# Kernel optimization log

Measured on AMD Instinct MI355X. Metric: run time of the kernel, lower is better.

The kernel has to match this reference:

```python
import jax, jax.numpy as jnp
import numpy as np

BATCH, T, D_MODEL, DIM = 8, 4096, 512, 512
R_MIN, R_MAX, MAX_PHASE = 0.0, 1.0, 6.28


def setup_inputs() -> dict:
    key = jax.random.key(0)
    ks = jax.random.split(key, 8)
    x = jax.random.normal(ks[0], (BATCH, T, D_MODEL), dtype=jnp.float32)
    h0 = jnp.zeros((BATCH, 1, DIM), dtype=jnp.float32)
    # nu_log / theta_log per the module's initializers
    u1 = jax.random.uniform(ks[1], (DIM,))
    nu_log = jnp.log(-0.5 * jnp.log(u1 * (R_MAX ** 2 - R_MIN ** 2) + R_MIN ** 2)).astype(jnp.float32)
    u2 = jax.random.uniform(ks[2], (DIM,))
    theta_log = jnp.log(MAX_PHASE * u2).astype(jnp.float32)
    # B ~ N(0,1)/sqrt(2*D_in), C ~ N(0,1)/sqrt(D_out)
    B_re = (jax.random.normal(ks[3], (D_MODEL, DIM)) / jnp.sqrt(2.0 * D_MODEL)).astype(jnp.float32)
    B_im = (jax.random.normal(ks[4], (D_MODEL, DIM)) / jnp.sqrt(2.0 * D_MODEL)).astype(jnp.float32)
    C_re = (jax.random.normal(ks[5], (DIM, D_MODEL)) / jnp.sqrt(float(D_MODEL))).astype(jnp.float32)
    C_im = (jax.random.normal(ks[6], (DIM, D_MODEL)) / jnp.sqrt(float(D_MODEL))).astype(jnp.float32)
    D_param = jax.random.normal(ks[7], (D_MODEL,)).astype(jnp.float32)
    # gamma_log = log(sqrt(1 - |Lambda|^2)) with Lambda from nu/theta
    diag_lambda = jnp.exp(-jnp.exp(nu_log) + 1j * jnp.exp(theta_log))
    gamma_log = jnp.log(jnp.sqrt(1.0 - jnp.abs(diag_lambda) ** 2)).astype(jnp.float32)
    return {"x": x, "h0": h0, "nu_log": nu_log, "theta_log": theta_log,
            "B_re": B_re, "B_im": B_im, "C_re": C_re, "C_im": C_im,
            "D_param": D_param, "gamma_log": gamma_log}


def _binary_op(ei, ej):
    a_i, b_i = ei
    a_j, b_j = ej
    return (a_j * a_i, a_j * b_i + b_j)


def reference(x, h0, nu_log, theta_log, B_re, B_im, C_re, C_im, D_param, gamma_log):
    B, T_len, _ = x.shape
    Lambda = jnp.exp(-jnp.exp(nu_log) + 1j * jnp.exp(theta_log))            # (N,) complex
    B_norm = (B_re + 1j * B_im) * jnp.exp(gamma_log)[None, :]               # (D,N) complex
    C = C_re + 1j * C_im                                                     # (N,D) complex
    # Input projection: Bu[b,t,n] = sum_d x[b,t,d] * B_norm[d,n]
    Bu = jnp.einsum('btd,dn->btn', x.astype(jnp.complex64), B_norm)
    Bu = jnp.concatenate([h0.astype(jnp.complex64), Bu], axis=1)             # (B,T+1,N)
    Lam = jnp.broadcast_to(Lambda, Bu.shape)                                 # (B,T+1,N)
    _, H = jax.lax.associative_scan(_binary_op, (Lam, Bu), axis=1)
    H = H[:, 1:]                                                             # (B,T,N)
    y = jnp.einsum('btn,nd->btd', H, C).real + D_param * x                   # (B,T,D)
    new_h = H[:, -1:]                                                        # (B,1,N) complex
    return (y, new_h)
```

## Files before the change

kernel.cpp:

```cpp
#include <hip/hip_runtime.h>

#define T_LEN 4096
#define DMODEL 512
#define DIM 512
#define NBATCH 8
#define MROWS (NBATCH * T_LEN)
#define NCHUNK 128
#define LCHUNK 32

typedef __attribute__((ext_vector_type(8))) short short8;
typedef __attribute__((ext_vector_type(4))) float float4v;

__device__ __forceinline__ ushort f2b(float f) {
    union { float fl; unsigned u; } v; v.fl = f;
    unsigned u = v.u;
    return (ushort)((u + 0x7FFFu + ((u >> 16) & 1u)) >> 16);
}
__device__ __forceinline__ float b2f(ushort u) {
    union { unsigned u; float f; } v; v.u = (unsigned)u << 16; return v.f;
}

__device__ __forceinline__ void glds16(const ushort* g, ushort* l) {
    __builtin_amdgcn_global_load_lds(
        (const __attribute__((address_space(1))) void*)g,
        (__attribute__((address_space(3))) void*)l, 16, 0, 0);
}

#define XBLK (MROWS * 512 / 4 / 256)
#define BBLK (1024 * 512 / 256)
#define CBLK (512 * 1024 / 256)

__global__ __launch_bounds__(256) void k_prep(const float* __restrict__ x,
                                              const float* __restrict__ B_re,
                                              const float* __restrict__ B_im,
                                              const float* __restrict__ gamma_log,
                                              const float* __restrict__ C_re,
                                              const float* __restrict__ C_im,
                                              ushort* __restrict__ Xb,
                                              ushort* __restrict__ BT,
                                              ushort* __restrict__ CT) {
    int bb = blockIdx.x;
    if (bb < XBLK) {
        int i = (bb * 256 + threadIdx.x) * 4;
        float4 v = *(const float4*)(x + i);
        ushort4 o;
        o.x = f2b(v.x); o.y = f2b(v.y); o.z = f2b(v.z); o.w = f2b(v.w);
        *(ushort4*)(Xb + i) = o;
    } else if (bb < XBLK + BBLK) {
        int idx = (bb - XBLK) * 256 + threadIdx.x;
        int n = idx >> 9;
        int d = idx & 511;
        float v;
        if (n < 512) v = B_re[d * 512 + n] * __expf(gamma_log[n]);
        else { int nn = n - 512; v = B_im[d * 512 + nn] * __expf(gamma_log[nn]); }
        BT[idx] = f2b(v);
    } else {
        int idx = (bb - XBLK - BBLK) * 256 + threadIdx.x;
        int d = idx >> 10;
        int k = idx & 1023;
        float v = (k < 512) ? C_re[k * 512 + d] : -C_im[(k - 512) * 512 + d];
        CT[idx] = f2b(v);
    }
}

template<int K, int MODE, int NBN>
__global__ __launch_bounds__(256) void k_gemm(
    const ushort* __restrict__ A, const ushort* __restrict__ Bt,
    ushort* __restrict__ oRe, ushort* __restrict__ oIm,
    float* __restrict__ y, const float* __restrict__ x, const float* __restrict__ Dp) {
    __shared__ ushort sA[128 * 64];
    __shared__ ushort sB[128 * 64];
    const int tid = threadIdx.x;
    const int L = blockIdx.x;
    const int xcd = L & 7;
    const int slot = L >> 3;
    const int m0 = (xcd * 32 + slot / NBN) * 128;
    const int n0 = (slot % NBN) * 128;
    const int wave = tid >> 6;
    const int lane = tid & 63;
    const int wm = (wave >> 1) * 64;
    const int wn = (wave & 1) * 64;
    const int lr = lane & 15;
    const int quad = lane >> 4;

    const int srow = lane >> 3;
    const int schunk = (lane & 7) ^ srow;
    const ushort* gA0 = A + (size_t)(m0 + wave * 32 + srow) * K + schunk * 8;
    const ushort* gB0 = Bt + (size_t)(n0 + wave * 32 + srow) * K + schunk * 8;

    float4v acc[4][4];
#pragma unroll
    for (int i = 0; i < 4; i++)
#pragma unroll
        for (int j = 0; j < 4; j++) {
            float4v z = {0.f, 0.f, 0.f, 0.f};
            acc[i][j] = z;
        }

    for (int k0 = 0; k0 < K; k0 += 64) {
        __syncthreads();
#pragma unroll
        for (int c = 0; c < 4; c++) {
            glds16(gA0 + (size_t)(c * 8) * K + k0, &sA[(wave * 32 + c * 8) * 64]);
            glds16(gB0 + (size_t)(c * 8) * K + k0, &sB[(wave * 32 + c * 8) * 64]);
        }
        __syncthreads();

#pragma unroll
        for (int kk = 0; kk < 2; kk++) {
            short8 af[4], bfr[4];
#pragma unroll
            for (int i = 0; i < 4; i++) {
                int row = wm + i * 16 + lr;
                af[i] = *(const short8*)&sA[row * 64 + (((kk * 4 + quad) ^ (row & 7)) * 8)];
            }
#pragma unroll
            for (int j = 0; j < 4; j++) {
                int row = wn + j * 16 + lr;
                bfr[j] = *(const short8*)&sB[row * 64 + (((kk * 4 + quad) ^ (row & 7)) * 8)];
            }
#pragma unroll
            for (int i = 0; i < 4; i++)
#pragma unroll
                for (int j = 0; j < 4; j++)
                    acc[i][j] = __builtin_amdgcn_mfma_f32_16x16x32_bf16(af[i], bfr[j], acc[i][j], 0, 0, 0);
        }
    }

#pragma unroll
    for (int i = 0; i < 4; i++) {
#pragma unroll
        for (int j = 0; j < 4; j++) {
            int gmb = m0 + wm + i * 16 + quad * 4;
            int gn = n0 + wn + j * 16 + lr;
#pragma unroll
            for (int r = 0; r < 4; r++) {
                float v = acc[i][j][r];
                int row = gmb + r;
                if (MODE == 1) {
                    if (gn < 512) oRe[(size_t)row * 512 + gn] = f2b(v);
                    else oIm[(size_t)row * 512 + (gn - 512)] = f2b(v);
                } else {
                    size_t o = (size_t)row * 512 + gn;
                    y[o] = v + Dp[gn] * x[o];
                }
            }
        }
    }
}


__device__ __forceinline__ void lambda_of(const float* nu_log, const float* theta_log,
                                          int n, float& lre, float& lim) {
    float e = __expf(nu_log[n]);
    float th = __expf(theta_log[n]);
    float rad = __expf(-e);
    float s, c;
    __sincosf(th, &s, &c);
    lre = rad * c;
    lim = rad * s;
}

__global__ __launch_bounds__(256) void k_scan1(const ushort* __restrict__ BuRe,
                                               const ushort* __restrict__ BuIm,
                                               const float* __restrict__ nu_log,
                                               const float* __restrict__ theta_log,
                                               float* __restrict__ cRe, float* __restrict__ cIm) {
    int n2 = threadIdx.x;
    int b = blockIdx.x >> 7;
    int c = blockIdx.x & 127;
    float lre0, lim0, lre1, lim1;
    lambda_of(nu_log, theta_log, 2 * n2, lre0, lim0);
    lambda_of(nu_log, theta_log, 2 * n2 + 1, lre1, lim1);
    float hr0 = 0.f, hi0 = 0.f, hr1 = 0.f, hi1 = 0.f;
    size_t base = ((size_t)b * T_LEN + (size_t)c * LCHUNK) * 512 + 2 * n2;
#pragma unroll 8
    for (int j = 0; j < LCHUNK; j++) {
        ushort2 ur = *(const ushort2*)(BuRe + base + (size_t)j * 512);
        ushort2 ui = *(const ushort2*)(BuIm + base + (size_t)j * 512);
        float br0 = b2f(ur.x), br1 = b2f(ur.y), bi0 = b2f(ui.x), bi1 = b2f(ui.y);
        float nr0 = lre0 * hr0 - lim0 * hi0 + br0;
        float ni0 = lre0 * hi0 + lim0 * hr0 + bi0;
        hr0 = nr0; hi0 = ni0;
        float nr1 = lre1 * hr1 - lim1 * hi1 + br1;
        float ni1 = lre1 * hi1 + lim1 * hr1 + bi1;
        hr1 = nr1; hi1 = ni1;
    }
    size_t co = ((size_t)b * NCHUNK + c) * 512 + 2 * n2;
    *(float2*)(cRe + co) = make_float2(hr0, hr1);
    *(float2*)(cIm + co) = make_float2(hi0, hi1);
}

__global__ __launch_bounds__(64) void k_scan2(const float* __restrict__ cRe,
                                              const float* __restrict__ cIm,
                                              const float* __restrict__ h0,
                                              const float* __restrict__ nu_log,
                                              const float* __restrict__ theta_log,
                                              float* __restrict__ pRe, float* __restrict__ pIm,
                                              float* __restrict__ newH, int newh_mode) {
    int idx = blockIdx.x * 64 + threadIdx.x;
    int b = idx >> 9;
    int n = idx & 511;
    float lre, lim;
    lambda_of(nu_log, theta_log, n, lre, lim);
    float Lr = lre, Li = lim;
#pragma unroll
    for (int s = 0; s < 5; s++) {
        float nr = Lr * Lr - Li * Li;
        float ni = 2.f * Lr * Li;
        Lr = nr; Li = ni;
    }
    float cr = h0[b * 512 + n];
    float ci = 0.f;
#pragma unroll 4
    for (int c = 0; c < NCHUNK; c++) {
        size_t o = ((size_t)b * NCHUNK + c) * 512 + n;
        pRe[o] = cr;
        pIm[o] = ci;
        float ar = cRe[o], ai = cIm[o];
        float nr = Lr * cr - Li * ci + ar;
        float ni = Lr * ci + Li * cr + ai;
        cr = nr; ci = ni;
    }
    size_t ci_idx = (size_t)b * 512 + n;
    if (newh_mode == 1) {
        newH[ci_idx] = cr;
        newH[(size_t)NBATCH * 512 + ci_idx] = ci;
    } else if (newh_mode == 2) {
        newH[ci_idx] = cr;
    } else {
        newH[ci_idx * 2] = cr;
        newH[ci_idx * 2 + 1] = ci;
    }
}

__global__ __launch_bounds__(256) void k_scan3(const ushort* __restrict__ BuRe,
                                               const ushort* __restrict__ BuIm,
                                               const float* __restrict__ pRe,
                                               const float* __restrict__ pIm,
                                               const float* __restrict__ nu_log,
                                               const float* __restrict__ theta_log,
                                               ushort* __restrict__ Hbf) {
    int n2 = threadIdx.x;
    int b = blockIdx.x >> 7;
    int c = blockIdx.x & 127;
    float lre0, lim0, lre1, lim1;
    lambda_of(nu_log, theta_log, 2 * n2, lre0, lim0);
    lambda_of(nu_log, theta_log, 2 * n2 + 1, lre1, lim1);
    size_t co = ((size_t)b * NCHUNK + c) * 512 + 2 * n2;
    float2 frv = *(const float2*)(pRe + co);
    float2 fiv = *(const float2*)(pIm + co);
    float fr0 = frv.x, fr1 = frv.y, fi0 = fiv.x, fi1 = fiv.y;
    float pr0 = lre0, pi0 = lim0, pr1 = lre1, pi1 = lim1;
    float hr0 = 0.f, hi0 = 0.f, hr1 = 0.f, hi1 = 0.f;
    size_t row0 = (size_t)b * T_LEN + (size_t)c * LCHUNK;
#pragma unroll 4
    for (int j = 0; j < LCHUNK; j++) {
        size_t base = (row0 + j) * 512 + 2 * n2;
        ushort2 ur = *(const ushort2*)(BuRe + base);
        ushort2 ui = *(const ushort2*)(BuIm + base);
        float br0 = b2f(ur.x), br1 = b2f(ur.y), bi0 = b2f(ui.x), bi1 = b2f(ui.y);
        float nr0 = lre0 * hr0 - lim0 * hi0 + br0;
        float ni0 = lre0 * hi0 + lim0 * hr0 + bi0;
        hr0 = nr0; hi0 = ni0;
        float nr1 = lre1 * hr1 - lim1 * hi1 + br1;
        float ni1 = lre1 * hi1 + lim1 * hr1 + bi1;
        hr1 = nr1; hi1 = ni1;
        float vr0 = hr0 + pr0 * fr0 - pi0 * fi0;
        float vi0 = hi0 + pr0 * fi0 + pi0 * fr0;
        float vr1 = hr1 + pr1 * fr1 - pi1 * fi1;
        float vi1 = hi1 + pr1 * fi1 + pi1 * fr1;
        size_t hrow = (row0 + j) * 1024;
        ushort2 wre, wim;
        wre.x = f2b(vr0); wre.y = f2b(vr1);
        wim.x = f2b(vi0); wim.y = f2b(vi1);
        *(ushort2*)(Hbf + hrow + 2 * n2) = wre;
        *(ushort2*)(Hbf + hrow + 512 + 2 * n2) = wim;
        float npr0 = pr0 * lre0 - pi0 * lim0;
        float npi0 = pr0 * lim0 + pi0 * lre0;
        pr0 = npr0; pi0 = npi0;
        float npr1 = pr1 * lre1 - pi1 * lim1;
        float npi1 = pr1 * lim1 + pi1 * lre1;
        pr1 = npr1; pi1 = npi1;
    }
}


extern "C" void kernel_launch(void* const* d_in, const int* in_sizes, int n_in,
                              void* d_out, int out_size, void* d_ws, size_t ws_size,
                              hipStream_t stream) {
    const float* x         = (const float*)d_in[0];
    const float* h0        = (const float*)d_in[1];
    const float* nu_log    = (const float*)d_in[2];
    const float* theta_log = (const float*)d_in[3];
    const float* B_re      = (const float*)d_in[4];
    const float* B_im      = (const float*)d_in[5];
    const float* C_re      = (const float*)d_in[6];
    const float* C_im      = (const float*)d_in[7];
    const float* D_param   = (const float*)d_in[8];
    const float* gamma_log = (const float*)d_in[9];

    char* ws = (char*)d_ws;
    size_t off = 0;
    ushort* Xb   = (ushort*)(ws + off); off += (size_t)MROWS * 512 * 2;
    ushort* BT   = (ushort*)(ws + off); off += (size_t)1024 * 512 * 2;
    ushort* CT   = (ushort*)(ws + off); off += (size_t)512 * 1024 * 2;
    ushort* BuRe = (ushort*)(ws + off); off += (size_t)MROWS * 512 * 2;
    ushort* BuIm = (ushort*)(ws + off); off += (size_t)MROWS * 512 * 2;
    ushort* Hbf  = (ushort*)(ws + off); off += (size_t)MROWS * 1024 * 2;
    float*  cRe  = (float*)(ws + off); off += (size_t)NBATCH * NCHUNK * 512 * 4;
    float*  cIm  = (float*)(ws + off); off += (size_t)NBATCH * NCHUNK * 512 * 4;
    float*  pRe  = (float*)(ws + off); off += (size_t)NBATCH * NCHUNK * 512 * 4;
    float*  pIm  = (float*)(ws + off); off += (size_t)NBATCH * NCHUNK * 512 * 4;

    float* y_out = (float*)d_out;
    float* newH  = (float*)d_out + (size_t)MROWS * 512;

    const int tail = out_size - MROWS * 512;
    int newh_mode = 0;
    if (tail == NBATCH * 512 * 2) newh_mode = 1;
    else if (tail == NBATCH * 512) newh_mode = 2;

    k_prep<<<dim3(XBLK + BBLK + CBLK), dim3(256), 0, stream>>>(
        x, B_re, B_im, gamma_log, C_re, C_im, Xb, BT, CT);

    k_gemm<512, 1, 8><<<dim3(2048), dim3(256), 0, stream>>>(
        Xb, BT, BuRe, BuIm, nullptr, nullptr, nullptr);

    k_scan1<<<dim3(NBATCH * NCHUNK), dim3(256), 0, stream>>>(BuRe, BuIm, nu_log, theta_log, cRe, cIm);
    k_scan2<<<dim3(NBATCH * 512 / 64), dim3(64), 0, stream>>>(cRe, cIm, h0, nu_log, theta_log, pRe, pIm, newH, newh_mode);
    k_scan3<<<dim3(NBATCH * NCHUNK), dim3(256), 0, stream>>>(BuRe, BuIm, pRe, pIm, nu_log, theta_log, Hbf);

    k_gemm<1024, 2, 4><<<dim3(1024), dim3(256), 0, stream>>>(
        Hbf, CT, nullptr, nullptr, y_out, x, D_param);
}
```

Measured before the change: 284.6 us.

## Double-buffer LDS tiles in bf16 GEMM to overlap global loads with MFMA

Turns the GEMM main loop into a two-stage LDS ping-pong. The async global-to-LDS copy of the next K-tile is issued before computing on the current tile, so load latency is meant to hide behind the MFMA work. Tile staging and compute are factored into helper functions, and one barrier per tile replaces the previous two. The cost is doubled LDS use per block, which may lower occupancy, and the loop assumes an even number of K-tiles.

```diff
diff --git a/kernel.cpp b/kernel.cpp
--- a/kernel.cpp
+++ b/kernel.cpp
@@ -63,13 +63,48 @@
     }
 }
 
+
+template<int K>
+__device__ __forceinline__ void stage_tile(const ushort* gA0, const ushort* gB0, int kt,
+                                           ushort* sAb, ushort* sBb, int wave) {
+#pragma unroll
+    for (int c = 0; c < 4; c++) {
+        glds16(gA0 + (size_t)(c * 8) * K + (size_t)kt * 64, &sAb[(wave * 32 + c * 8) * 64]);
+        glds16(gB0 + (size_t)(c * 8) * K + (size_t)kt * 64, &sBb[(wave * 32 + c * 8) * 64]);
+    }
+}
+
+__device__ __forceinline__ void compute_tile(const ushort* sAb, const ushort* sBb,
+                                             int wm, int wn, int lr, int quad,
+                                             float4v acc[4][4]) {
+#pragma unroll
+    for (int kk = 0; kk < 2; kk++) {
+        short8 af[4], bfr[4];
+#pragma unroll
+        for (int i = 0; i < 4; i++) {
+            int row = wm + i * 16 + lr;
+            af[i] = *(const short8*)&sAb[row * 64 + (((kk * 4 + quad) ^ (row & 7)) * 8)];
+        }
+#pragma unroll
+        for (int j = 0; j < 4; j++) {
+            int row = wn + j * 16 + lr;
+            bfr[j] = *(const short8*)&sBb[row * 64 + (((kk * 4 + quad) ^ (row & 7)) * 8)];
+        }
+#pragma unroll
+        for (int i = 0; i < 4; i++)
+#pragma unroll
+            for (int j = 0; j < 4; j++)
+                acc[i][j] = __builtin_amdgcn_mfma_f32_16x16x32_bf16(af[i], bfr[j], acc[i][j], 0, 0, 0);
+    }
+}
+
 template<int K, int MODE, int NBN>
 __global__ __launch_bounds__(256) void k_gemm(
     const ushort* __restrict__ A, const ushort* __restrict__ Bt,
     ushort* __restrict__ oRe, ushort* __restrict__ oIm,
     float* __restrict__ y, const float* __restrict__ x, const float* __restrict__ Dp) {
-    __shared__ ushort sA[128 * 64];
-    __shared__ ushort sB[128 * 64];
+    __shared__ ushort sA[2][128 * 64];
+    __shared__ ushort sB[2][128 * 64];
     const int tid = threadIdx.x;
     const int L = blockIdx.x;
     const int xcd = L & 7;
@@ -97,34 +132,20 @@
             acc[i][j] = z;
         }
 
-    for (int k0 = 0; k0 < K; k0 += 64) {
+    const int NT = K / 64;
+
+    stage_tile<K>(gA0, gB0, 0, &sA[0][0], &sB[0][0], wave);
+    __syncthreads();
+
+    for (int t = 0; t < NT; t += 2) {
+        stage_tile<K>(gA0, gB0, t + 1, &sA[1][0], &sB[1][0], wave);
+        compute_tile(&sA[0][0], &sB[0][0], wm, wn, lr, quad, acc);
         __syncthreads();
-#pragma unroll
-        for (int c = 0; c < 4; c++) {
-            glds16(gA0 + (size_t)(c * 8) * K + k0, &sA[(wave * 32 + c * 8) * 64]);
-            glds16(gB0 + (size_t)(c * 8) * K + k0, &sB[(wave * 32 + c * 8) * 64]);
-        }
+
+        if (t + 2 < NT)
+            stage_tile<K>(gA0, gB0, t + 2, &sA[0][0], &sB[0][0], wave);
+        compute_tile(&sA[1][0], &sB[1][0], wm, wn, lr, quad, acc);
         __syncthreads();
-
-#pragma unroll
-        for (int kk = 0; kk < 2; kk++) {
-            short8 af[4], bfr[4];
-#pragma unroll
-            for (int i = 0; i < 4; i++) {
-                int row = wm + i * 16 + lr;
-                af[i] = *(const short8*)&sA[row * 64 + (((kk * 4 + quad) ^ (row & 7)) * 8)];
-            }
-#pragma unroll
-            for (int j = 0; j < 4; j++) {
-                int row = wn + j * 16 + lr;
-                bfr[j] = *(const short8*)&sB[row * 64 + (((kk * 4 + quad) ^ (row & 7)) * 8)];
-            }
-#pragma unroll
-            for (int i = 0; i < 4; i++)
-#pragma unroll
-                for (int j = 0; j < 4; j++)
-                    acc[i][j] = __builtin_amdgcn_mfma_f32_16x16x32_bf16(af[i], bfr[j], acc[i][j], 0, 0, 0);
-        }
     }
 
 #pragma unroll
```

After: 287.2 us. Within noise of the previous version (+0.9%).

## Fuse fp32-to-bf16 conversion of x into input-projection GEMM with prefetching

Applied to the files above, without the earlier changes.

Removes the separate pass that converted x to a bf16 workspace and instead loads fp32 x directly in the first GEMM, converting to bf16 in registers before storing to LDS. The B operand is double-buffered in LDS and the next A tile is prefetched into registers while the current tile computes. This avoids writing and re-reading a large bf16 copy of x, at the cost of extra fp32 global reads per block and conversion work inside the GEMM loop.

```diff
diff --git a/kernel.cpp b/kernel.cpp
--- a/kernel.cpp
+++ b/kernel.cpp
@@ -26,28 +26,19 @@
         (__attribute__((address_space(3))) void*)l, 16, 0, 0);
 }
 
-#define XBLK (MROWS * 512 / 4 / 256)
 #define BBLK (1024 * 512 / 256)
 #define CBLK (512 * 1024 / 256)
 
-__global__ __launch_bounds__(256) void k_prep(const float* __restrict__ x,
-                                              const float* __restrict__ B_re,
+__global__ __launch_bounds__(256) void k_prep(const float* __restrict__ B_re,
                                               const float* __restrict__ B_im,
                                               const float* __restrict__ gamma_log,
                                               const float* __restrict__ C_re,
                                               const float* __restrict__ C_im,
-                                              ushort* __restrict__ Xb,
                                               ushort* __restrict__ BT,
                                               ushort* __restrict__ CT) {
     int bb = blockIdx.x;
-    if (bb < XBLK) {
-        int i = (bb * 256 + threadIdx.x) * 4;
-        float4 v = *(const float4*)(x + i);
-        ushort4 o;
-        o.x = f2b(v.x); o.y = f2b(v.y); o.z = f2b(v.z); o.w = f2b(v.w);
-        *(ushort4*)(Xb + i) = o;
-    } else if (bb < XBLK + BBLK) {
-        int idx = (bb - XBLK) * 256 + threadIdx.x;
+    if (bb < BBLK) {
+        int idx = bb * 256 + threadIdx.x;
         int n = idx >> 9;
         int d = idx & 511;
         float v;
@@ -55,7 +46,7 @@
         else { int nn = n - 512; v = B_im[d * 512 + nn] * __expf(gamma_log[nn]); }
         BT[idx] = f2b(v);
     } else {
-        int idx = (bb - XBLK - BBLK) * 256 + threadIdx.x;
+        int idx = (bb - BBLK) * 256 + threadIdx.x;
         int d = idx >> 10;
         int k = idx & 1023;
         float v = (k < 512) ? C_re[k * 512 + d] : -C_im[(k - 512) * 512 + d];
@@ -63,19 +54,141 @@
     }
 }
 
-template<int K, int MODE, int NBN>
-__global__ __launch_bounds__(256) void k_gemm(
+
+__device__ __forceinline__ void compute_tile(const ushort* sAb, const ushort* sBb,
+                                             int wm, int wn, int lr, int quad,
+                                             float4v acc[4][4]) {
+#pragma unroll
+    for (int kk = 0; kk < 2; kk++) {
+        short8 af[4], bfr[4];
+#pragma unroll
+        for (int i = 0; i < 4; i++) {
+            int row = wm + i * 16 + lr;
+            af[i] = *(const short8*)&sAb[row * 64 + (((kk * 4 + quad) ^ (row & 7)) * 8)];
+        }
+#pragma unroll
+        for (int j = 0; j < 4; j++) {
+            int row = wn + j * 16 + lr;
+            bfr[j] = *(const short8*)&sBb[row * 64 + (((kk * 4 + quad) ^ (row & 7)) * 8)];
+        }
+#pragma unroll
+        for (int i = 0; i < 4; i++)
+#pragma unroll
+            for (int j = 0; j < 4; j++)
+                acc[i][j] = __builtin_amdgcn_mfma_f32_16x16x32_bf16(af[i], bfr[j], acc[i][j], 0, 0, 0);
+    }
+}
+
+__global__ __launch_bounds__(256) void k_gemm1(
+    const float* __restrict__ X, const ushort* __restrict__ Bt,
+    ushort* __restrict__ oRe, ushort* __restrict__ oIm) {
+    const int K = 512;
+    const int NT = K / 64;
+    __shared__ ushort sA[128 * 64];
+    __shared__ ushort sB[2][128 * 64];
+    const int tid = threadIdx.x;
+    const int L = blockIdx.x;
+    const int xcd = L & 7;
+    const int slot = L >> 3;
+    const int m0 = (xcd * 32 + slot / 8) * 128;
+    const int n0 = (slot % 8) * 128;
+    const int wave = tid >> 6;
+    const int lane = tid & 63;
+    const int wm = (wave >> 1) * 64;
+    const int wn = (wave & 1) * 64;
+    const int lr = lane & 15;
+    const int quad = lane >> 4;
+
+    const int srow = lane >> 3;
+    const int schunk = (lane & 7) ^ srow;
+    const float*  gX0 = X  + (size_t)(m0 + wave * 32 + srow) * 512 + schunk * 8;
+    const ushort* gB0 = Bt + (size_t)(n0 + wave * 32 + srow) * K + schunk * 8;
+
+    float4v acc[4][4];
+#pragma unroll
+    for (int i = 0; i < 4; i++)
+#pragma unroll
+        for (int j = 0; j < 4; j++) {
+            float4v z = {0.f, 0.f, 0.f, 0.f};
+            acc[i][j] = z;
+        }
+
+    float4 fa[4][2];
+#pragma unroll
+    for (int c = 0; c < 4; c++) {
+        const float* p = gX0 + (size_t)(c * 8) * 512;
+        fa[c][0] = *(const float4*)p;
+        fa[c][1] = *(const float4*)(p + 4);
+        glds16(gB0 + (size_t)(c * 8) * K, &sB[0][(wave * 32 + c * 8) * 64]);
+    }
+#pragma unroll
+    for (int c = 0; c < 4; c++) {
+        short8 o;
+        o[0] = (short)f2b(fa[c][0].x); o[1] = (short)f2b(fa[c][0].y);
+        o[2] = (short)f2b(fa[c][0].z); o[3] = (short)f2b(fa[c][0].w);
+        o[4] = (short)f2b(fa[c][1].x); o[5] = (short)f2b(fa[c][1].y);
+        o[6] = (short)f2b(fa[c][1].z); o[7] = (short)f2b(fa[c][1].w);
+        *(short8*)&sA[(wave * 32 + c * 8) * 64 + lane * 8] = o;
+    }
+    __syncthreads();
+
+    for (int t = 0; t < NT; t++) {
+        const bool more = (t + 1 < NT);
+        if (more) {
+#pragma unroll
+            for (int c = 0; c < 4; c++) {
+                const float* p = gX0 + (size_t)(c * 8) * 512 + (t + 1) * 64;
+                fa[c][0] = *(const float4*)p;
+                fa[c][1] = *(const float4*)(p + 4);
+                glds16(gB0 + (size_t)(c * 8) * K + (t + 1) * 64,
+                       &sB[(t + 1) & 1][(wave * 32 + c * 8) * 64]);
+            }
+        }
+        compute_tile(sA, &sB[t & 1][0], wm, wn, lr, quad, acc);
+        __syncthreads();
+        if (more) {
+#pragma unroll
+            for (int c = 0; c < 4; c++) {
+                short8 o;
+                o[0] = (short)f2b(fa[c][0].x); o[1] = (short)f2b(fa[c][0].y);
+                o[2] = (short)f2b(fa[c][0].z); o[3] = (short)f2b(fa[c][0].w);
+                o[4] = (short)f2b(fa[c][1].x); o[5] = (short)f2b(fa[c][1].y);
+                o[6] = (short)f2b(fa[c][1].z); o[7] = (short)f2b(fa[c][1].w);
+                *(short8*)&sA[(wave * 32 + c * 8) * 64 + lane * 8] = o;
+            }
+            __syncthreads();
+        }
+    }
+
+#pragma unroll
+    for (int i = 0; i < 4; i++) {
+#pragma unroll
+        for (int j = 0; j < 4; j++) {
+            int gmb = m0 + wm + i * 16 + quad * 4;
+            int gn = n0 + wn + j * 16 + lr;
+#pragma unroll
+            for (int r = 0; r < 4; r++) {
+                float v = acc[i][j][r];
+                int row = gmb + r;
+                if (gn < 512) oRe[(size_t)row * 512 + gn] = f2b(v);
+                else oIm[(size_t)row * 512 + (gn - 512)] = f2b(v);
+            }
+        }
+    }
+}
+
+__global__ __launch_bounds__(256) void k_gemm2(
     const ushort* __restrict__ A, const ushort* __restrict__ Bt,
-    ushort* __restrict__ oRe, ushort* __restrict__ oIm,
     float* __restrict__ y, const float* __restrict__ x, const float* __restrict__ Dp) {
+    const int K = 1024;
     __shared__ ushort sA[128 * 64];
     __shared__ ushort sB[128 * 64];
     const int tid = threadIdx.x;
     const int L = blockIdx.x;
     const int xcd = L & 7;
     const int slot = L >> 3;
-    const int m0 = (xcd * 32 + slot / NBN) * 128;
-    const int n0 = (slot % NBN) * 128;
+    const int m0 = (xcd * 32 + slot / 4) * 128;
+    const int n0 = (slot % 4) * 128;
     const int wave = tid >> 6;
     const int lane = tid & 63;
     const int wm = (wave >> 1) * 64;
@@ -105,26 +218,7 @@
             glds16(gB0 + (size_t)(c * 8) * K + k0, &sB[(wave * 32 + c * 8) * 64]);
         }
         __syncthreads();
-
-#pragma unroll
-        for (int kk = 0; kk < 2; kk++) {
-            short8 af[4], bfr[4];
-#pragma unroll
-            for (int i = 0; i < 4; i++) {
-                int row = wm + i * 16 + lr;
-                af[i] = *(const short8*)&sA[row * 64 + (((kk * 4 + quad) ^ (row & 7)) * 8)];
-            }
-#pragma unroll
-            for (int j = 0; j < 4; j++) {
-                int row = wn + j * 16 + lr;
-                bfr[j] = *(const short8*)&sB[row * 64 + (((kk * 4 + quad) ^ (row & 7)) * 8)];
-            }
-#pragma unroll
-            for (int i = 0; i < 4; i++)
-#pragma unroll
-                for (int j = 0; j < 4; j++)
-                    acc[i][j] = __builtin_amdgcn_mfma_f32_16x16x32_bf16(af[i], bfr[j], acc[i][j], 0, 0, 0);
-        }
+        compute_tile(sA, sB, wm, wn, lr, quad, acc);
     }
 
 #pragma unroll
@@ -137,13 +231,8 @@
             for (int r = 0; r < 4; r++) {
                 float v = acc[i][j][r];
                 int row = gmb + r;
-                if (MODE == 1) {
-                    if (gn < 512) oRe[(size_t)row * 512 + gn] = f2b(v);
-                    else oIm[(size_t)row * 512 + (gn - 512)] = f2b(v);
-                } else {
-                    size_t o = (size_t)row * 512 + gn;
-                    y[o] = v + Dp[gn] * x[o];
-                }
+                size_t o = (size_t)row * 512 + gn;
+                y[o] = v + Dp[gn] * x[o];
             }
         }
     }
@@ -302,7 +391,6 @@
 
     char* ws = (char*)d_ws;
     size_t off = 0;
-    ushort* Xb   = (ushort*)(ws + off); off += (size_t)MROWS * 512 * 2;
     ushort* BT   = (ushort*)(ws + off); off += (size_t)1024 * 512 * 2;
     ushort* CT   = (ushort*)(ws + off); off += (size_t)512 * 1024 * 2;
     ushort* BuRe = (ushort*)(ws + off); off += (size_t)MROWS * 512 * 2;
@@ -321,16 +409,14 @@
     if (tail == NBATCH * 512 * 2) newh_mode = 1;
     else if (tail == NBATCH * 512) newh_mode = 2;
 
-    k_prep<<<dim3(XBLK + BBLK + CBLK), dim3(256), 0, stream>>>(
-        x, B_re, B_im, gamma_log, C_re, C_im, Xb, BT, CT);
-
-    k_gemm<512, 1, 8><<<dim3(2048), dim3(256), 0, stream>>>(
-        Xb, BT, BuRe, BuIm, nullptr, nullptr, nullptr);
+    k_prep<<<dim3(BBLK + CBLK), dim3(256), 0, stream>>>(
+        B_re, B_im, gamma_log, C_re, C_im, BT, CT);
+
+    k_gemm1<<<dim3(2048), dim3(256), 0, stream>>>(x, BT, BuRe, BuIm);
 
     k_scan1<<<dim3(NBATCH * NCHUNK), dim3(256), 0, stream>>>(BuRe, BuIm, nu_log, theta_log, cRe, cIm);
     k_scan2<<<dim3(NBATCH * 512 / 64), dim3(64), 0, stream>>>(cRe, cIm, h0, nu_log, theta_log, pRe, pIm, newH, newh_mode);
     k_scan3<<<dim3(NBATCH * NCHUNK), dim3(256), 0, stream>>>(BuRe, BuIm, pRe, pIm, nu_log, theta_log, Hbf);
 
-    k_gemm<1024, 2, 4><<<dim3(1024), dim3(256), 0, stream>>>(
-        Hbf, CT, nullptr, nullptr, y_out, x, D_param);
-}
+    k_gemm2<<<dim3(1024), dim3(256), 0, stream>>>(Hbf, CT, y_out, x, D_param);
+}
```

Result: slower. 305.0 us (+7.2%).

## Fuse chunk-carry scan into the final scan pass and tile weight transposes

Applied to the files above, without the earlier changes.

Removes the serial k_scan2 kernel by having each chunk block recompute its incoming carry: it walks the chunk-summary states of all earlier chunks, applying Lambda^32, then runs the intra-chunk scan. The last chunk also writes new_h. This cuts a kernel launch, a low-parallelism serial pass and the pRe/pIm round trip. In exchange it adds redundant work that grows with chunk index, up to 127 steps for the last chunk. Separately, the B/C weight transposes now go through a 64x65 shared-memory tile so both global reads and writes are coalesced.

```diff
diff --git a/kernel.cpp b/kernel.cpp
--- a/kernel.cpp
+++ b/kernel.cpp
@@ -27,8 +27,7 @@
 }
 
 #define XBLK (MROWS * 512 / 4 / 256)
-#define BBLK (1024 * 512 / 256)
-#define CBLK (512 * 1024 / 256)
+#define TBLK 256
 
 __global__ __launch_bounds__(256) void k_prep(const float* __restrict__ x,
                                               const float* __restrict__ B_re,
@@ -39,6 +38,7 @@
                                               ushort* __restrict__ Xb,
                                               ushort* __restrict__ BT,
                                               ushort* __restrict__ CT) {
+    __shared__ float T[64][65];
     int bb = blockIdx.x;
     if (bb < XBLK) {
         int i = (bb * 256 + threadIdx.x) * 4;
@@ -46,20 +46,32 @@
         ushort4 o;
         o.x = f2b(v.x); o.y = f2b(v.y); o.z = f2b(v.z); o.w = f2b(v.w);
         *(ushort4*)(Xb + i) = o;
-    } else if (bb < XBLK + BBLK) {
-        int idx = (bb - XBLK) * 256 + threadIdx.x;
-        int n = idx >> 9;
-        int d = idx & 511;
-        float v;
-        if (n < 512) v = B_re[d * 512 + n] * __expf(gamma_log[n]);
-        else { int nn = n - 512; v = B_im[d * 512 + nn] * __expf(gamma_log[nn]); }
-        BT[idx] = f2b(v);
-    } else {
-        int idx = (bb - XBLK - BBLK) * 256 + threadIdx.x;
-        int d = idx >> 10;
-        int k = idx & 1023;
-        float v = (k < 512) ? C_re[k * 512 + d] : -C_im[(k - 512) * 512 + d];
-        CT[idx] = f2b(v);
+        return;
+    }
+    int tb = bb - XBLK;
+    int mat = tb >> 6;
+    int tile = tb & 63;
+    int r0 = (tile >> 3) * 64;
+    int c0 = (tile & 7) * 64;
+    const float* IN = (mat == 0) ? B_re : (mat == 1) ? B_im : (mat == 2) ? C_re : C_im;
+    int lr_ = threadIdx.x & 63;
+    int lc  = threadIdx.x >> 6;
+#pragma unroll
+    for (int p = 0; p < 16; p++)
+        T[4 * p + lc][lr_] = IN[(size_t)(c0 + 4 * p + lc) * 512 + r0 + lr_];
+    __syncthreads();
+#pragma unroll
+    for (int p = 0; p < 16; p++) {
+        int rr = 4 * p + lc;
+        int r = r0 + rr;
+        float v = T[lr_][rr];
+        if (mat <= 1) {
+            v *= __expf(gamma_log[r]);
+            BT[(size_t)(mat * 512 + r) * 512 + c0 + lr_] = f2b(v);
+        } else {
+            if (mat == 3) v = -v;
+            CT[(size_t)r * 1024 + (mat - 2) * 512 + c0 + lr_] = f2b(v);
+        }
     }
 }
 
@@ -191,66 +203,60 @@
     *(float2*)(cIm + co) = make_float2(hi0, hi1);
 }
 
-__global__ __launch_bounds__(64) void k_scan2(const float* __restrict__ cRe,
-                                              const float* __restrict__ cIm,
-                                              const float* __restrict__ h0,
-                                              const float* __restrict__ nu_log,
-                                              const float* __restrict__ theta_log,
-                                              float* __restrict__ pRe, float* __restrict__ pIm,
-                                              float* __restrict__ newH, int newh_mode) {
-    int idx = blockIdx.x * 64 + threadIdx.x;
-    int b = idx >> 9;
-    int n = idx & 511;
-    float lre, lim;
-    lambda_of(nu_log, theta_log, n, lre, lim);
-    float Lr = lre, Li = lim;
-#pragma unroll
-    for (int s = 0; s < 5; s++) {
-        float nr = Lr * Lr - Li * Li;
-        float ni = 2.f * Lr * Li;
-        Lr = nr; Li = ni;
-    }
-    float cr = h0[b * 512 + n];
-    float ci = 0.f;
-#pragma unroll 4
-    for (int c = 0; c < NCHUNK; c++) {
-        size_t o = ((size_t)b * NCHUNK + c) * 512 + n;
-        pRe[o] = cr;
-        pIm[o] = ci;
-        float ar = cRe[o], ai = cIm[o];
-        float nr = Lr * cr - Li * ci + ar;
-        float ni = Lr * ci + Li * cr + ai;
-        cr = nr; ci = ni;
-    }
-    size_t ci_idx = (size_t)b * 512 + n;
-    if (newh_mode == 1) {
-        newH[ci_idx] = cr;
-        newH[(size_t)NBATCH * 512 + ci_idx] = ci;
-    } else if (newh_mode == 2) {
-        newH[ci_idx] = cr;
-    } else {
-        newH[ci_idx * 2] = cr;
-        newH[ci_idx * 2 + 1] = ci;
-    }
-}
-
-__global__ __launch_bounds__(256) void k_scan3(const ushort* __restrict__ BuRe,
+__global__ __launch_bounds__(256) void k_scanB(const ushort* __restrict__ BuRe,
                                                const ushort* __restrict__ BuIm,
-                                               const float* __restrict__ pRe,
-                                               const float* __restrict__ pIm,
+                                               const float* __restrict__ cRe,
+                                               const float* __restrict__ cIm,
+                                               const float* __restrict__ h0,
                                                const float* __restrict__ nu_log,
                                                const float* __restrict__ theta_log,
-                                               ushort* __restrict__ Hbf) {
+                                               ushort* __restrict__ Hbf,
+                                               float* __restrict__ newH, int newh_mode) {
     int n2 = threadIdx.x;
     int b = blockIdx.x >> 7;
     int c = blockIdx.x & 127;
     float lre0, lim0, lre1, lim1;
     lambda_of(nu_log, theta_log, 2 * n2, lre0, lim0);
     lambda_of(nu_log, theta_log, 2 * n2 + 1, lre1, lim1);
-    size_t co = ((size_t)b * NCHUNK + c) * 512 + 2 * n2;
-    float2 frv = *(const float2*)(pRe + co);
-    float2 fiv = *(const float2*)(pIm + co);
-    float fr0 = frv.x, fr1 = frv.y, fi0 = fiv.x, fi1 = fiv.y;
+    float Lr0 = lre0, Li0 = lim0, Lr1 = lre1, Li1 = lim1;
+#pragma unroll
+    for (int s = 0; s < 5; s++) {
+        float a0 = Lr0 * Lr0 - Li0 * Li0, q0 = 2.f * Lr0 * Li0; Lr0 = a0; Li0 = q0;
+        float a1 = Lr1 * Lr1 - Li1 * Li1, q1 = 2.f * Lr1 * Li1; Lr1 = a1; Li1 = q1;
+    }
+    float fr0 = h0[b * 512 + 2 * n2], fi0 = 0.f;
+    float fr1 = h0[b * 512 + 2 * n2 + 1], fi1 = 0.f;
+    size_t cb = (size_t)b * NCHUNK * 512 + 2 * n2;
+#pragma unroll 4
+    for (int j = 0; j < c; j++) {
+        float2 ar = *(const float2*)(cRe + cb + (size_t)j * 512);
+        float2 ai = *(const float2*)(cIm + cb + (size_t)j * 512);
+        float nr0 = Lr0 * fr0 - Li0 * fi0 + ar.x;
+        float ni0 = Lr0 * fi0 + Li0 * fr0 + ai.x;
+        fr0 = nr0; fi0 = ni0;
+        float nr1 = Lr1 * fr1 - Li1 * fi1 + ar.y;
+        float ni1 = Lr1 * fi1 + Li1 * fr1 + ai.y;
+        fr1 = nr1; fi1 = ni1;
+    }
+    if (c == NCHUNK - 1) {
+        float2 ar = *(const float2*)(cRe + cb + (size_t)(NCHUNK - 1) * 512);
+        float2 ai = *(const float2*)(cIm + cb + (size_t)(NCHUNK - 1) * 512);
+        float cr0 = Lr0 * fr0 - Li0 * fi0 + ar.x;
+        float ci0 = Lr0 * fi0 + Li0 * fr0 + ai.x;
+        float cr1 = Lr1 * fr1 - Li1 * fi1 + ar.y;
+        float ci1 = Lr1 * fi1 + Li1 * fr1 + ai.y;
+        size_t i0 = (size_t)b * 512 + 2 * n2;
+        if (newh_mode == 1) {
+            newH[i0] = cr0; newH[i0 + 1] = cr1;
+            newH[(size_t)NBATCH * 512 + i0] = ci0;
+            newH[(size_t)NBATCH * 512 + i0 + 1] = ci1;
+        } else if (newh_mode == 2) {
+            newH[i0] = cr0; newH[i0 + 1] = cr1;
+        } else {
+            newH[i0 * 2] = cr0; newH[i0 * 2 + 1] = ci0;
+            newH[(i0 + 1) * 2] = cr1; newH[(i0 + 1) * 2 + 1] = ci1;
+        }
+    }
     float pr0 = lre0, pi0 = lim0, pr1 = lre1, pi1 = lim1;
     float hr0 = 0.f, hi0 = 0.f, hr1 = 0.f, hi1 = 0.f;
     size_t row0 = (size_t)b * T_LEN + (size_t)c * LCHUNK;
@@ -310,8 +316,6 @@
     ushort* Hbf  = (ushort*)(ws + off); off += (size_t)MROWS * 1024 * 2;
     float*  cRe  = (float*)(ws + off); off += (size_t)NBATCH * NCHUNK * 512 * 4;
     float*  cIm  = (float*)(ws + off); off += (size_t)NBATCH * NCHUNK * 512 * 4;
-    float*  pRe  = (float*)(ws + off); off += (size_t)NBATCH * NCHUNK * 512 * 4;
-    float*  pIm  = (float*)(ws + off); off += (size_t)NBATCH * NCHUNK * 512 * 4;
 
     float* y_out = (float*)d_out;
     float* newH  = (float*)d_out + (size_t)MROWS * 512;
@@ -321,15 +325,15 @@
     if (tail == NBATCH * 512 * 2) newh_mode = 1;
     else if (tail == NBATCH * 512) newh_mode = 2;
 
-    k_prep<<<dim3(XBLK + BBLK + CBLK), dim3(256), 0, stream>>>(
+    k_prep<<<dim3(XBLK + TBLK), dim3(256), 0, stream>>>(
         x, B_re, B_im, gamma_log, C_re, C_im, Xb, BT, CT);
 
     k_gemm<512, 1, 8><<<dim3(2048), dim3(256), 0, stream>>>(
         Xb, BT, BuRe, BuIm, nullptr, nullptr, nullptr);
 
     k_scan1<<<dim3(NBATCH * NCHUNK), dim3(256), 0, stream>>>(BuRe, BuIm, nu_log, theta_log, cRe, cIm);
-    k_scan2<<<dim3(NBATCH * 512 / 64), dim3(64), 0, stream>>>(cRe, cIm, h0, nu_log, theta_log, pRe, pIm, newH, newh_mode);
-    k_scan3<<<dim3(NBATCH * NCHUNK), dim3(256), 0, stream>>>(BuRe, BuIm, pRe, pIm, nu_log, theta_log, Hbf);
+    k_scanB<<<dim3(NBATCH * NCHUNK), dim3(256), 0, stream>>>(
+        BuRe, BuIm, cRe, cIm, h0, nu_log, theta_log, Hbf, newH, newh_mode);
 
     k_gemm<1024, 2, 4><<<dim3(1024), dim3(256), 0, stream>>>(
         Hbf, CT, nullptr, nullptr, y_out, x, D_param);
```

Result: no change. 285.7 us (+0.4%).
